# Performance work log

Hardware: AMD Instinct MI355X
Metric: run time of the kernel (lower is better)

## Reference

```python
import jax, jax.numpy as jnp
import numpy as np

B, LAT, CIN, W, K, F = 16, 512, 512, 4096, 3, 512

def setup_inputs() -> dict:
    key = jax.random.key(0)
    k1, k2, k3, k4 = jax.random.split(key, 4)
    latent = jax.random.normal(k1, (B, LAT), jnp.float32)
    content = jax.random.normal(k2, (B, CIN, W), jnp.float32)
    # glorot_uniform for affine weight
    lim = np.sqrt(6.0 / (LAT + CIN))
    affine_w = jax.random.uniform(k3, (LAT, CIN), jnp.float32, -lim, lim)
    affine_b = jnp.zeros((1, CIN), jnp.float32)
    # he_normal for conv kernel (fan_in = K*CIN)
    kernel_w = jax.random.normal(k4, (K, CIN, F), jnp.float32) * np.sqrt(2.0 / (K * CIN))
    kernel_b = jnp.zeros((1, F, 1), jnp.float32)
    return {"latent": latent, "content": content, "affine_w": affine_w,
            "affine_b": affine_b, "kernel_w": kernel_w, "kernel_b": kernel_b}

def reference(latent, content, affine_w, affine_b, kernel_w, kernel_b):
    # style affine: [B, CIN]
    affine = latent @ affine_w + affine_b
    # demod scale per (b, f): 1/sqrt(sum_{k,c} (kernel[k,c,f]*affine[b,c])^2 + 1e-8)
    demod = jax.lax.rsqrt(jnp.einsum('kcf,bc->bf', kernel_w * kernel_w,
                                     affine * affine) + 1e-8)
    # modulate input instead of per-sample weights (mathematically identical,
    # avoids batch-as-groups grouped conv): x[b,c,w] = content * affine[b,c]
    x = content * affine[:, :, None]
    # shared-kernel conv1d, NCW / SAME; filter layout [K, CIN, F] == HIO
    y = jax.lax.conv_general_dilated(
        x, kernel_w, window_strides=(1,), padding='SAME',
        dimension_numbers=('NCH', 'HIO', 'NCH'))
    y = y * demod[:, :, None] + kernel_b  # [B, F, W]
    return jnp.where(y >= 0, y, 0.2 * y)  # leaky_relu(0.2)
```

## Files before the change

### kernel.cpp

```cpp
#include <hip/hip_runtime.h>
#include <hip/hip_bf16.h>

#define Bn   16
#define LATn 512
#define Cn   512
#define Wn   4096
#define Fn   512

using bf16x8 = __attribute__((ext_vector_type(8))) short;
using f32x4  = __attribute__((ext_vector_type(4))) float;

__device__ __forceinline__ unsigned short f2bf(float x) {
    union { float f; unsigned int u; } v; v.f = x;
    unsigned int r = v.u + 0x7fffu + ((v.u >> 16) & 1u);
    return (unsigned short)(r >> 16);
}

__device__ __forceinline__ void gload_lds16(const void* g, void* l) {
    __builtin_amdgcn_global_load_lds(
        (const __attribute__((address_space(1))) unsigned int*)g,
        (__attribute__((address_space(3))) unsigned int*)l, 16, 0, 0);
}

__global__ void k_affine(const float* __restrict__ latent,
                         const float* __restrict__ aw,
                         const float* __restrict__ ab,
                         float* __restrict__ affine,
                         float* __restrict__ zbuf) {
    if (blockIdx.x == 0 && blockIdx.y == 0 && threadIdx.x < 16)
        zbuf[threadIdx.x] = 0.f;
    const int c = blockIdx.x * 256 + threadIdx.x;
    const int b = blockIdx.y;
    float s0 = 0.f, s1 = 0.f;
    for (int l = 0; l < LATn; l += 2) {
        s0 = fmaf(latent[b * LATn + l],     aw[(size_t)l * Cn + c],       s0);
        s1 = fmaf(latent[b * LATn + l + 1], aw[(size_t)(l + 1) * Cn + c], s1);
    }
    affine[b * Cn + c] = s0 + s1 + ab[c];
}

__global__ void k_qsum(const float* __restrict__ kw, float* __restrict__ Q) {
    const int i = (blockIdx.x * 256 + threadIdx.x) * 4;
    const float4 a = *(const float4*)&kw[i];
    const float4 b = *(const float4*)&kw[Cn * Fn + i];
    const float4 c = *(const float4*)&kw[2 * Cn * Fn + i];
    float4 q;
    q.x = a.x * a.x + b.x * b.x + c.x * c.x;
    q.y = a.y * a.y + b.y * b.y + c.y * c.y;
    q.z = a.z * a.z + b.z * b.z + c.z * c.z;
    q.w = a.w * a.w + b.w * b.w + c.w * c.w;
    *(float4*)&Q[i] = q;
}

__global__ void k_demod2(const float* __restrict__ Q,
                         const float* __restrict__ affine,
                         float* __restrict__ demod) {
    const int f = blockIdx.x * 256 + threadIdx.x;
    const int b = blockIdx.y;
    float s0 = 0.f, s1 = 0.f, s2 = 0.f, s3 = 0.f;
    for (int c = 0; c < Cn; c += 4) {
        const float a0 = affine[b * Cn + c + 0];
        const float a1 = affine[b * Cn + c + 1];
        const float a2 = affine[b * Cn + c + 2];
        const float a3 = affine[b * Cn + c + 3];
        s0 = fmaf(a0 * a0, Q[(size_t)(c + 0) * Fn + f], s0);
        s1 = fmaf(a1 * a1, Q[(size_t)(c + 1) * Fn + f], s1);
        s2 = fmaf(a2 * a2, Q[(size_t)(c + 2) * Fn + f], s2);
        s3 = fmaf(a3 * a3, Q[(size_t)(c + 3) * Fn + f], s3);
    }
    demod[b * Fn + f] = rsqrtf(s0 + s1 + s2 + s3 + 1e-8f);
}

__global__ void k_tk(const float* __restrict__ kw, unsigned short* __restrict__ kt) {
    __shared__ float lds[32][65];
    const int t  = threadIdx.x;
    const int k  = blockIdx.z;
    const int c0 = blockIdx.x * 32;
    const int f0 = blockIdx.y * 64;
    #pragma unroll
    for (int i = 0; i < 8; ++i) {
        int e = t + 256 * i; int c = e >> 6; int f = e & 63;
        lds[c][f] = kw[((size_t)(k * Cn + c0 + c)) * Fn + f0 + f];
    }
    __syncthreads();
    #pragma unroll
    for (int i = 0; i < 8; ++i) {
        int e = t + 256 * i; int f = e >> 5; int c = e & 31;
        kt[((size_t)(k * Fn + f0 + f)) * Cn + c0 + c] = f2bf(lds[c][f]);
    }
}

__global__ void k_tx(const float* __restrict__ content,
                     const float* __restrict__ affine,
                     unsigned short* __restrict__ xt) {
    __shared__ unsigned short lds[64][72];
    const int t  = threadIdx.x;
    const int b  = blockIdx.z;
    const int c0 = blockIdx.y * 64;
    const int w0 = blockIdx.x * 64;
    #pragma unroll
    for (int i = 0; i < 4; ++i) {
        int e = t + 256 * i;
        int c = e >> 4;
        int w4 = (e & 15) * 4;
        float4 v = *(const float4*)&content[((size_t)(b * Cn + c0 + c)) * Wn + w0 + w4];
        float a = affine[b * Cn + c0 + c];
        int wx = w4 ^ ((c >> 3) << 3);
        unsigned short p[4] = {f2bf(v.x * a), f2bf(v.y * a), f2bf(v.z * a), f2bf(v.w * a)};
        *(uint2*)&lds[c][wx] = *(const uint2*)p;
    }
    __syncthreads();
    #pragma unroll
    for (int i = 0; i < 2; ++i) {
        int e = t + 256 * i;
        int w  = e >> 3;
        int q  = e & 7;
        int c8 = q * 8;
        int wx = w ^ (q << 3);
        unsigned short tmp[8];
        #pragma unroll
        for (int j = 0; j < 8; ++j) tmp[j] = lds[c8 + j][wx];
        *(uint4*)&xt[((size_t)b * Wn + w0 + w) * Cn + c0 + c8] = *(uint4*)tmp;
    }
}

#define BM 256
#define BN 256
#define BK 32
#define KBYTES (3 * BM * BK * 2)
#define BUFB   (KBYTES + BN * BK * 2)
#define SMEMB  (2 * BUFB + 2 * Cn * 2)

__device__ __forceinline__ void stage_step(
    const unsigned short* __restrict__ kt, const unsigned short* __restrict__ xt,
    char* dst, int t, int f0, int w0, int b, int c0s) {
    #pragma unroll
    for (int i = 0; i < 6; ++i) {
        const int Q = i * 512 + t;
        const int k = Q >> 10;
        const int r = (Q >> 2) & 255;
        const int j = (Q & 3) ^ ((r >> 1) & 3);
        gload_lds16(&kt[((size_t)(k * Fn + f0 + r)) * Cn + c0s + j * 8],
                    dst + (size_t)Q * 16);
    }
    #pragma unroll
    for (int i = 0; i < 2; ++i) {
        const int Q = i * 512 + t;
        const int r = Q >> 2;
        const int j = (Q & 3) ^ ((r >> 1) & 3);
        gload_lds16(&xt[((size_t)b * Wn + w0 + r) * Cn + c0s + j * 8],
                    dst + KBYTES + (size_t)Q * 16);
    }
}

extern __shared__ __align__(16) char smem[];

__global__ __launch_bounds__(512, 2)
void k_conv(const unsigned short* __restrict__ kt,
            const unsigned short* __restrict__ xt,
            const float* __restrict__ demod,
            const float* __restrict__ kb,
            const float* __restrict__ zbuf,
            float* __restrict__ y) {
    const int t  = threadIdx.x;
    const int w0 = blockIdx.x * BN;
    const int f0 = blockIdx.y * BM;
    const int b  = blockIdx.z;

    const int wave = t >> 6;
    const int lane = t & 63;
    const int wm   = wave >> 2;
    const int wn   = wave & 3;
    const int l15  = lane & 15;
    const int lhi  = lane >> 4;

    unsigned short* halo = (unsigned short*)(smem + 2 * BUFB);

    f32x4 acc[8][4];
    #pragma unroll
    for (int m = 0; m < 8; ++m)
        #pragma unroll
        for (int n = 0; n < 4; ++n)
            #pragma unroll
            for (int r = 0; r < 4; ++r)
                acc[m][n][r] = 0.f;

    if (t < 128) {
        const int h  = t >> 6;
        const int j  = t & 63;
        const int wg = h ? (w0 + BN) : (w0 - 1);
        const unsigned short* src = ((unsigned)wg < (unsigned)Wn)
            ? &xt[((size_t)b * Wn + wg) * Cn + j * 8]
            : (const unsigned short*)zbuf;
        gload_lds16(src, halo + (size_t)t * 8);
    }
    stage_step(kt, xt, smem, t, f0, w0, b, 0);
    __syncthreads();

    int cur = 0;
    for (int cc = 0; cc < Cn / BK; ++cc) {
        char* bufc = smem + cur * BUFB;
        const unsigned short* ka = (const unsigned short*)bufc;
        const unsigned short* xa = (const unsigned short*)(bufc + KBYTES);
        if (cc < Cn / BK - 1)
            stage_step(kt, xt, smem + (cur ^ 1) * BUFB, t, f0, w0, b, (cc + 1) * BK);
        const int c0 = cc * BK;

        #pragma unroll
        for (int k = 0; k < 3; ++k) {
            bf16x8 af[8];
            #pragma unroll
            for (int m = 0; m < 8; ++m) {
                const int r = wm * 128 + m * 16 + l15;
                af[m] = *(const bf16x8*)(ka + (k * 256 + r) * 32 + (lhi ^ ((r >> 1) & 3)) * 8);
            }
            bf16x8 bv[4];
            #pragma unroll
            for (int n = 0; n < 4; ++n) {
                const int rl = wn * 64 + n * 16 + l15 + k - 1;
                const unsigned short* bp;
                if (k == 0 && n == 0) {
                    bp = (rl < 0) ? (halo + c0 + lhi * 8)
                                  : (xa + rl * 32 + (lhi ^ ((rl >> 1) & 3)) * 8);
                } else if (k == 2 && n == 3) {
                    bp = (rl > 255) ? (halo + 512 + c0 + lhi * 8)
                                    : (xa + rl * 32 + (lhi ^ ((rl >> 1) & 3)) * 8);
                } else {
                    bp = xa + rl * 32 + (lhi ^ ((rl >> 1) & 3)) * 8;
                }
                bv[n] = *(const bf16x8*)bp;
            }
            __builtin_amdgcn_s_setprio(1);
            #pragma unroll
            for (int n = 0; n < 4; ++n)
                #pragma unroll
                for (int m = 0; m < 8; ++m)
                    acc[m][n] = __builtin_amdgcn_mfma_f32_16x16x32_bf16(af[m], bv[n], acc[m][n], 0, 0, 0);
            __builtin_amdgcn_s_setprio(0);
        }
        __syncthreads();
        cur ^= 1;
    }

    #pragma unroll
    for (int m = 0; m < 8; ++m) {
        const int fb = f0 + wm * 128 + m * 16 + lhi * 4;
        const float4 dmv = *(const float4*)&demod[b * Fn + fb];
        const float4 kbv = *(const float4*)&kb[fb];
        const float dmf[4] = {dmv.x, dmv.y, dmv.z, dmv.w};
        const float kbf[4] = {kbv.x, kbv.y, kbv.z, kbv.w};
        #pragma unroll
        for (int n = 0; n < 4; ++n) {
            const int w = w0 + wn * 64 + n * 16 + l15;
            #pragma unroll
            for (int r = 0; r < 4; ++r) {
                float v = fmaf(acc[m][n][r], dmf[r], kbf[r]);
                v = (v >= 0.f) ? v : 0.2f * v;
                y[((size_t)(b * Fn + fb + r)) * Wn + w] = v;
            }
        }
    }
}

extern "C" void kernel_launch(void* const* d_in, const int* in_sizes, int n_in,
                              void* d_out, int out_size, void* d_ws, size_t ws_size,
                              hipStream_t stream) {
    const float* latent  = (const float*)d_in[0];
    const float* content = (const float*)d_in[1];
    const float* aw      = (const float*)d_in[2];
    const float* ab      = (const float*)d_in[3];
    const float* kw      = (const float*)d_in[4];
    const float* kb      = (const float*)d_in[5];
    float* y = (float*)d_out;

    char* ws = (char*)d_ws;
    float*          affine = (float*)(ws);
    float*          demod  = (float*)(ws + 32768);
    float*          zbuf   = (float*)(ws + 65536);
    float*          Q      = (float*)(ws + 131072);
    unsigned short* kt     = (unsigned short*)(ws + 131072);
    unsigned short* xt     = (unsigned short*)(ws + 2u * 1024u * 1024u);
    if (ws_size < 2u * 1024u * 1024u + (size_t)Bn * Wn * Cn * 2u) return;

    hipFuncSetAttribute((const void*)k_conv,
                        hipFuncAttributeMaxDynamicSharedMemorySize, SMEMB);

    k_affine<<<dim3(Cn / 256, Bn),          256, 0, stream>>>(latent, aw, ab, affine, zbuf);
    k_qsum  <<<dim3(Cn * Fn / 1024),        256, 0, stream>>>(kw, Q);
    k_demod2<<<dim3(Fn / 256, Bn),          256, 0, stream>>>(Q, affine, demod);
    k_tk    <<<dim3(Cn / 32, Fn / 64, 3),   256, 0, stream>>>(kw, kt);
    k_tx    <<<dim3(Wn / 64, Cn / 64, Bn),  256, 0, stream>>>(content, affine, xt);
    k_conv  <<<dim3(Wn / BN, Fn / BM, Bn),  512, SMEMB, stream>>>(kt, xt, demod, kb, zbuf, y);
}
```

Measured before the change: 175.8 us.

## Split conv prefetch per kernel plane with fine-grained vmcnt waits; parallelize affine/demod reductions

The conv main loop now issues next-stage global-to-LDS loads in pieces, one kernel plane per k-phase. Each phase waits with explicit s_waitcnt vmcnt and s_barrier instead of a full __syncthreads, so loads and MFMA work overlap more finely. The launch bound drops to one workgroup per SIMD to allow more registers. The affine and demod kernels split their reductions across four thread groups with an LDS combine, which launches more blocks. The hand-counted vmcnt values and barriers risk races if the counts are wrong, and the occupancy hint change could reduce latency hiding.

```diff
diff --git a/kernel.cpp b/kernel.cpp
--- a/kernel.cpp
+++ b/kernel.cpp
@@ -29,14 +29,20 @@
                          float* __restrict__ zbuf) {
     if (blockIdx.x == 0 && blockIdx.y == 0 && threadIdx.x < 16)
         zbuf[threadIdx.x] = 0.f;
-    const int c = blockIdx.x * 256 + threadIdx.x;
-    const int b = blockIdx.y;
-    float s0 = 0.f, s1 = 0.f;
-    for (int l = 0; l < LATn; l += 2) {
-        s0 = fmaf(latent[b * LATn + l],     aw[(size_t)l * Cn + c],       s0);
-        s1 = fmaf(latent[b * LATn + l + 1], aw[(size_t)(l + 1) * Cn + c], s1);
-    }
-    affine[b * Cn + c] = s0 + s1 + ab[c];
+    __shared__ float red[4][64];
+    const int t  = threadIdx.x;
+    const int cl = t & 63, lq = t >> 6;
+    const int c  = blockIdx.x * 64 + cl;
+    const int b  = blockIdx.y;
+    float s = 0.f;
+    #pragma unroll 4
+    for (int l = lq * 128; l < lq * 128 + 128; ++l)
+        s = fmaf(latent[b * LATn + l], aw[(size_t)l * Cn + c], s);
+    red[lq][cl] = s;
+    __syncthreads();
+    if (t < 64)
+        affine[b * Cn + blockIdx.x * 64 + t] =
+            red[0][t] + red[1][t] + red[2][t] + red[3][t] + ab[blockIdx.x * 64 + t];
 }
 
 __global__ void k_qsum(const float* __restrict__ kw, float* __restrict__ Q) {
@@ -55,20 +61,22 @@
 __global__ void k_demod2(const float* __restrict__ Q,
                          const float* __restrict__ affine,
                          float* __restrict__ demod) {
-    const int f = blockIdx.x * 256 + threadIdx.x;
-    const int b = blockIdx.y;
-    float s0 = 0.f, s1 = 0.f, s2 = 0.f, s3 = 0.f;
-    for (int c = 0; c < Cn; c += 4) {
-        const float a0 = affine[b * Cn + c + 0];
-        const float a1 = affine[b * Cn + c + 1];
-        const float a2 = affine[b * Cn + c + 2];
-        const float a3 = affine[b * Cn + c + 3];
-        s0 = fmaf(a0 * a0, Q[(size_t)(c + 0) * Fn + f], s0);
-        s1 = fmaf(a1 * a1, Q[(size_t)(c + 1) * Fn + f], s1);
-        s2 = fmaf(a2 * a2, Q[(size_t)(c + 2) * Fn + f], s2);
-        s3 = fmaf(a3 * a3, Q[(size_t)(c + 3) * Fn + f], s3);
-    }
-    demod[b * Fn + f] = rsqrtf(s0 + s1 + s2 + s3 + 1e-8f);
+    __shared__ float red[4][64];
+    const int t  = threadIdx.x;
+    const int fl = t & 63, cq = t >> 6;
+    const int f  = blockIdx.x * 64 + fl;
+    const int b  = blockIdx.y;
+    float s = 0.f;
+    #pragma unroll 4
+    for (int c = cq * 128; c < cq * 128 + 128; ++c) {
+        const float a = affine[b * Cn + c];
+        s = fmaf(a * a, Q[(size_t)c * Fn + f], s);
+    }
+    red[cq][fl] = s;
+    __syncthreads();
+    if (t < 64)
+        demod[b * Fn + blockIdx.x * 64 + t] =
+            rsqrtf(red[0][t] + red[1][t] + red[2][t] + red[3][t] + 1e-8f);
 }
 
 __global__ void k_tk(const float* __restrict__ kw, unsigned short* __restrict__ kt) {
@@ -131,31 +139,47 @@
 #define BUFB   (KBYTES + BN * BK * 2)
 #define SMEMB  (2 * BUFB + 2 * Cn * 2)
 
-__device__ __forceinline__ void stage_step(
-    const unsigned short* __restrict__ kt, const unsigned short* __restrict__ xt,
-    char* dst, int t, int f0, int w0, int b, int c0s) {
-    #pragma unroll
-    for (int i = 0; i < 6; ++i) {
-        const int Q = i * 512 + t;
-        const int k = Q >> 10;
-        const int r = (Q >> 2) & 255;
-        const int j = (Q & 3) ^ ((r >> 1) & 3);
-        gload_lds16(&kt[((size_t)(k * Fn + f0 + r)) * Cn + c0s + j * 8],
-                    dst + (size_t)Q * 16);
-    }
-    #pragma unroll
-    for (int i = 0; i < 2; ++i) {
-        const int Q = i * 512 + t;
-        const int r = Q >> 2;
-        const int j = (Q & 3) ^ ((r >> 1) & 3);
-        gload_lds16(&xt[((size_t)b * Wn + w0 + r) * Cn + c0s + j * 8],
-                    dst + KBYTES + (size_t)Q * 16);
-    }
-}
-
 extern __shared__ __align__(16) char smem[];
 
-__global__ __launch_bounds__(512, 2)
+#define ISSUE_XT(dst, c0s) { \
+    _Pragma("unroll") for (int i_ = 0; i_ < 2; ++i_) { \
+        const int Q_ = i_ * 512 + t; \
+        const int r_ = Q_ >> 2; \
+        const int j_ = (Q_ & 3) ^ ((r_ >> 1) & 3); \
+        gload_lds16(&xt[((size_t)b * Wn + w0 + r_) * Cn + (c0s) + j_ * 8], \
+                    (dst) + KBYTES + (size_t)Q_ * 16); } }
+
+#define ISSUE_PLANE(dst, c0s, P) { \
+    _Pragma("unroll") for (int i_ = 0; i_ < 2; ++i_) { \
+        const int Q_ = i_ * 512 + t; \
+        const int r_ = Q_ >> 2; \
+        const int j_ = (Q_ & 3) ^ ((r_ >> 1) & 3); \
+        gload_lds16(&kt[((size_t)((P) * Fn + f0 + r_)) * Cn + (c0s) + j_ * 8], \
+                    (dst) + (size_t)((P) * 1024 + Q_) * 16); } }
+
+#define PHASE(K, VM, ...) { \
+    asm volatile("s_waitcnt vmcnt(" #VM ")" ::: "memory"); \
+    asm volatile("s_barrier" ::: "memory"); \
+    bf16x8 af[8]; bf16x8 bv[4]; \
+    _Pragma("unroll") for (int m_ = 0; m_ < 8; ++m_) { \
+        const int r_ = wm * 128 + m_ * 16 + l15; \
+        af[m_] = *(const bf16x8*)(ka + ((K) * 256 + r_) * 32 + (lhi ^ ((r_ >> 1) & 3)) * 8); } \
+    _Pragma("unroll") for (int n_ = 0; n_ < 4; ++n_) { \
+        const int rl_ = wn * 64 + n_ * 16 + l15 + (K) - 1; \
+        const unsigned short* bp_ = xa + rl_ * 32 + (lhi ^ ((rl_ >> 1) & 3)) * 8; \
+        if ((K) == 0 && n_ == 0 && rl_ < 0)   bp_ = halo + c0 + lhi * 8; \
+        if ((K) == 2 && n_ == 3 && rl_ > 255) bp_ = halo + 512 + c0 + lhi * 8; \
+        bv[n_] = *(const bf16x8*)bp_; } \
+    __VA_ARGS__; \
+    asm volatile("s_waitcnt lgkmcnt(0)" ::: "memory"); \
+    __builtin_amdgcn_sched_barrier(0); \
+    __builtin_amdgcn_s_setprio(1); \
+    _Pragma("unroll") for (int n_ = 0; n_ < 4; ++n_) \
+        _Pragma("unroll") for (int m_ = 0; m_ < 8; ++m_) \
+            acc[m_][n_] = __builtin_amdgcn_mfma_f32_16x16x32_bf16(af[m_], bv[n_], acc[m_][n_], 0, 0, 0); \
+    __builtin_amdgcn_s_setprio(0); }
+
+__global__ __launch_bounds__(512, 1)
 void k_conv(const unsigned short* __restrict__ kt,
             const unsigned short* __restrict__ xt,
             const float* __restrict__ demod,
@@ -187,58 +211,28 @@
 
     if (t < 128) {
         const int h  = t >> 6;
-        const int j  = t & 63;
         const int wg = h ? (w0 + BN) : (w0 - 1);
         const unsigned short* src = ((unsigned)wg < (unsigned)Wn)
-            ? &xt[((size_t)b * Wn + wg) * Cn + j * 8]
+            ? &xt[((size_t)b * Wn + wg) * Cn + (t & 63) * 8]
             : (const unsigned short*)zbuf;
         gload_lds16(src, halo + (size_t)t * 8);
     }
-    stage_step(kt, xt, smem, t, f0, w0, b, 0);
-    __syncthreads();
+    ISSUE_XT(smem, 0);
+    ISSUE_PLANE(smem, 0, 0);
+    ISSUE_PLANE(smem, 0, 1);
+    ISSUE_PLANE(smem, 0, 2);
 
     int cur = 0;
     for (int cc = 0; cc < Cn / BK; ++cc) {
-        char* bufc = smem + cur * BUFB;
-        const unsigned short* ka = (const unsigned short*)bufc;
-        const unsigned short* xa = (const unsigned short*)(bufc + KBYTES);
-        if (cc < Cn / BK - 1)
-            stage_step(kt, xt, smem + (cur ^ 1) * BUFB, t, f0, w0, b, (cc + 1) * BK);
+        const unsigned short* ka = (const unsigned short*)(smem + cur * BUFB);
+        const unsigned short* xa = ka + 3 * BM * BK;
+        char* nbuf = smem + (cur ^ 1) * BUFB;
         const int c0 = cc * BK;
-
-        #pragma unroll
-        for (int k = 0; k < 3; ++k) {
-            bf16x8 af[8];
-            #pragma unroll
-            for (int m = 0; m < 8; ++m) {
-                const int r = wm * 128 + m * 16 + l15;
-                af[m] = *(const bf16x8*)(ka + (k * 256 + r) * 32 + (lhi ^ ((r >> 1) & 3)) * 8);
-            }
-            bf16x8 bv[4];
-            #pragma unroll
-            for (int n = 0; n < 4; ++n) {
-                const int rl = wn * 64 + n * 16 + l15 + k - 1;
-                const unsigned short* bp;
-                if (k == 0 && n == 0) {
-                    bp = (rl < 0) ? (halo + c0 + lhi * 8)
-                                  : (xa + rl * 32 + (lhi ^ ((rl >> 1) & 3)) * 8);
-                } else if (k == 2 && n == 3) {
-                    bp = (rl > 255) ? (halo + 512 + c0 + lhi * 8)
-                                    : (xa + rl * 32 + (lhi ^ ((rl >> 1) & 3)) * 8);
-                } else {
-                    bp = xa + rl * 32 + (lhi ^ ((rl >> 1) & 3)) * 8;
-                }
-                bv[n] = *(const bf16x8*)bp;
-            }
-            __builtin_amdgcn_s_setprio(1);
-            #pragma unroll
-            for (int n = 0; n < 4; ++n)
-                #pragma unroll
-                for (int m = 0; m < 8; ++m)
-                    acc[m][n] = __builtin_amdgcn_mfma_f32_16x16x32_bf16(af[m], bv[n], acc[m][n], 0, 0, 0);
-            __builtin_amdgcn_s_setprio(0);
-        }
-        __syncthreads();
+        const int c1 = c0 + BK;
+        const bool pf = cc < Cn / BK - 1;
+        PHASE(0, 4, if (pf) { ISSUE_XT(nbuf, c1); ISSUE_PLANE(nbuf, c1, 0); });
+        PHASE(1, 6, if (pf) { ISSUE_PLANE(nbuf, c1, 1); });
+        PHASE(2, 6, if (pf) { ISSUE_PLANE(nbuf, c1, 2); });
         cur ^= 1;
     }
 
@@ -285,9 +279,9 @@
     hipFuncSetAttribute((const void*)k_conv,
                         hipFuncAttributeMaxDynamicSharedMemorySize, SMEMB);
 
-    k_affine<<<dim3(Cn / 256, Bn),          256, 0, stream>>>(latent, aw, ab, affine, zbuf);
+    k_affine<<<dim3(Cn / 64, Bn),           256, 0, stream>>>(latent, aw, ab, affine, zbuf);
     k_qsum  <<<dim3(Cn * Fn / 1024),        256, 0, stream>>>(kw, Q);
-    k_demod2<<<dim3(Fn / 256, Bn),          256, 0, stream>>>(Q, affine, demod);
+    k_demod2<<<dim3(Fn / 64, Bn),           256, 0, stream>>>(Q, affine, demod);
     k_tk    <<<dim3(Cn / 32, Fn / 64, 3),   256, 0, stream>>>(kw, kt);
     k_tx    <<<dim3(Wn / 64, Cn / 64, Bn),  256, 0, stream>>>(content, affine, xt);
     k_conv  <<<dim3(Wn / BN, Fn / BM, Bn),  512, SMEMB, stream>>>(kt, xt, demod, kb, zbuf, y);
```

Result: faster. 167.1 us (-5.0%).
